# Kernel optimization log

Measured on AMD Instinct MI355X. Metric: run time of the kernel, lower is better.

## Reference

```python
import jax, jax.numpy as jnp
import numpy as np

BLOCK_SIZE = 64
WINDOW_SIZE = 256  # local_window pattern: each query block attends to blocks within the window
NEG_INF = -1e30


def setup_inputs() -> dict:
    key = jax.random.key(0)
    kq, kk, kv = jax.random.split(key, 3)
    B, S, H, D = 2, 4096, 16, 64
    q = jax.random.normal(kq, (B, S, H, D), dtype=jnp.float32)
    k = jax.random.normal(kk, (B, S, H, D), dtype=jnp.float32)
    v = jax.random.normal(kv, (B, S, H, D), dtype=jnp.float32)
    return {"q": q, "k": k, "v": v}


def _block_sparse_attn(q, k, v):
    # q, k, v: [B, S, H, D]
    B, S, H, D = q.shape
    bs = BLOCK_SIZE
    N = S // bs                      # number of blocks
    W = WINDOW_SIZE // bs            # window in blocks (4)
    half = W // 2
    offsets = jnp.arange(-half, half + 1)          # [K] neighbor offsets, K = W+1 = 5
    K = offsets.shape[0]

    i = jnp.arange(N)
    j = i[:, None] + offsets[None, :]              # [N, K] neighbor block ids
    valid = (j >= 0) & (j < N)                     # boundary mask
    jc = jnp.clip(j, 0, N - 1)

    # reshape into blocks: [B, H, N, bs, D]
    qb = q.reshape(B, N, bs, H, D).transpose(0, 3, 1, 2, 4)
    kb = k.reshape(B, N, bs, H, D).transpose(0, 3, 1, 2, 4)
    vb = v.reshape(B, N, bs, H, D).transpose(0, 3, 1, 2, 4)

    # gather only the active (neighbor) key/value blocks: [B, H, N, K, bs, D]
    kn = kb[:, :, jc]
    vn = vb[:, :, jc]

    scale = 1.0 / jnp.sqrt(jnp.asarray(D, dtype=q.dtype))
    # block scores: [B, H, N, bs, K, bs]
    scores = jnp.einsum('bhnqd,bhnkcd->bhnqkc', qb, kn) * scale
    scores = jnp.where(valid[None, None, :, None, :, None], scores, NEG_INF)

    # softmax over the union of active key blocks for each query block
    scores = scores.reshape(B, H, N, bs, K * bs)
    attn = jax.nn.softmax(scores, axis=-1)
    out = jnp.einsum('bhnqe,bhned->bhnqd', attn, vn.reshape(B, H, N, K * bs, D))

    # back to [B, S, H, D]
    return out.transpose(0, 2, 3, 1, 4).reshape(B, S, H, D)


def reference(q, k, v):
    return _block_sparse_attn(q, k, v)
```

## Files before the change

kernel.cpp:

```cpp
#include <hip/hip_runtime.h>

#define S_DIM 4096
#define H_DIM 16
#define D_DIM 64
#define N_BLK 64
#define NEG_INF_F (-1e30f)
#define QSCALE 0.125f

typedef __attribute__((ext_vector_type(4))) float f32x4;
typedef __attribute__((ext_vector_type(8))) short s16x8;
typedef __attribute__((ext_vector_type(4))) unsigned int u32x4;
typedef __attribute__((ext_vector_type(2))) unsigned int u32x2;

__device__ __forceinline__ unsigned int fbits(float f) {
    return __builtin_bit_cast(unsigned int, f);
}
__device__ __forceinline__ unsigned int pkbf(float a, float b) {
    return __builtin_amdgcn_perm(fbits(b) + 0x8000u, fbits(a) + 0x8000u, 0x07060302u);
}

__global__ __launch_bounds__(256, 2) void bsattn_kernel(
    const float* __restrict__ qg, const float* __restrict__ kg,
    const float* __restrict__ vg, float* __restrict__ outg)
{
    __shared__ unsigned int lds_vt[D_DIM * 256];

    const int tid  = threadIdx.x;
    const int w    = tid >> 6;
    const int lane = tid & 63;
    const int quad = lane >> 4;
    const int l16  = lane & 15;

    const int b  = blockIdx.z;
    const int h  = blockIdx.y;
    const int n0 = blockIdx.x << 2;
    const int n  = n0 + w;

    s16x8 bq[4][2];
#pragma unroll
    for (int qt = 0; qt < 4; ++qt) {
        const size_t qrow = ((size_t)(b * S_DIM + n * 64 + qt * 16 + l16) * H_DIM + h) * D_DIM;
#pragma unroll
        for (int hh = 0; hh < 2; ++hh) {
            const float4* qp = reinterpret_cast<const float4*>(qg + qrow + hh * 32 + quad * 8);
            float4 f0 = qp[0];
            float4 f1 = qp[1];
            u32x4 u;
            u.x = pkbf(f0.x * QSCALE, f0.y * QSCALE);
            u.y = pkbf(f0.z * QSCALE, f0.w * QSCALE);
            u.z = pkbf(f1.x * QSCALE, f1.y * QSCALE);
            u.w = pkbf(f1.z * QSCALE, f1.w * QSCALE);
            bq[qt][hh] = __builtin_bit_cast(s16x8, u);
        }
    }

    {
        const int jt = tid >> 5;
        const int sp = tid & 31;
        const int jv = n0 - 2 + jt;
        if (jv >= 0 && jv < N_BLK) {
            const float* v0p = vg + ((size_t)(b * S_DIM + jv * 64 + 2 * sp) * H_DIM + h) * D_DIM;
            const float* v1p = v0p + H_DIM * D_DIM;
            const int craw = jt * 64 + 2 * sp;
#pragma unroll
            for (int ch = 0; ch < 4; ++ch) {
                const int d0 = ch * 16;
                const float4* ap = reinterpret_cast<const float4*>(v0p + d0);
                const float4* bp = reinterpret_cast<const float4*>(v1p + d0);
                float4 a0 = ap[0], a1 = ap[1], a2 = ap[2], a3 = ap[3];
                float4 b0 = bp[0], b1 = bp[1], b2 = bp[2], b3 = bp[3];
                float av[16] = {a0.x,a0.y,a0.z,a0.w, a1.x,a1.y,a1.z,a1.w,
                                a2.x,a2.y,a2.z,a2.w, a3.x,a3.y,a3.z,a3.w};
                float bv[16] = {b0.x,b0.y,b0.z,b0.w, b1.x,b1.y,b1.z,b1.w,
                                b2.x,b2.y,b2.z,b2.w, b3.x,b3.y,b3.z,b3.w};
#pragma unroll
                for (int i = 0; i < 16; ++i) {
                    const int d = d0 + i;
                    lds_vt[d * 256 + (((craw + 8 * d) & 511) >> 1)] = pkbf(av[i], bv[i]);
                }
            }
        }
    }

    f32x4 o[4][4];
    float m_run[4], l_run[4];
#pragma unroll
    for (int qt = 0; qt < 4; ++qt) {
        m_run[qt] = NEG_INF_F; l_run[qt] = 0.f;
#pragma unroll
        for (int dt = 0; dt < 4; ++dt) o[qt][dt] = (f32x4){0.f, 0.f, 0.f, 0.f};
    }

    __syncthreads();

    const int colb = quad * 4 + 8 * l16;

    for (int t = 0; t < 5; ++t) {
        const int j = n - 2 + t;
        if (j < 0 || j >= N_BLK) continue;
        const int ji = w + t;

        float4 kf[4][2][2];
#pragma unroll
        for (int kt = 0; kt < 4; ++kt) {
            const size_t krow = ((size_t)(b * S_DIM + j * 64 + kt * 16 + l16) * H_DIM + h) * D_DIM + quad * 8;
#pragma unroll
            for (int hh = 0; hh < 2; ++hh) {
                const float4* kp = reinterpret_cast<const float4*>(kg + krow + hh * 32);
                kf[kt][hh][0] = kp[0];
                kf[kt][hh][1] = kp[1];
            }
        }
        s16x8 kbf[4][2];
#pragma unroll
        for (int kt = 0; kt < 4; ++kt)
#pragma unroll
            for (int hh = 0; hh < 2; ++hh) {
                u32x4 u;
                u.x = pkbf(kf[kt][hh][0].x, kf[kt][hh][0].y);
                u.y = pkbf(kf[kt][hh][0].z, kf[kt][hh][0].w);
                u.z = pkbf(kf[kt][hh][1].x, kf[kt][hh][1].y);
                u.w = pkbf(kf[kt][hh][1].z, kf[kt][hh][1].w);
                kbf[kt][hh] = __builtin_bit_cast(s16x8, u);
            }

        s16x8 pa[4][2];
#pragma unroll
        for (int qt = 0; qt < 4; ++qt) {
            f32x4 sa[4];
#pragma unroll
            for (int kt = 0; kt < 4; ++kt) {
                f32x4 z = {0.f, 0.f, 0.f, 0.f};
                f32x4 a0 = __builtin_amdgcn_mfma_f32_16x16x32_bf16(kbf[kt][0], bq[qt][0], z, 0, 0, 0);
                sa[kt]   = __builtin_amdgcn_mfma_f32_16x16x32_bf16(kbf[kt][1], bq[qt][1], a0, 0, 0, 0);
            }
            float mx = NEG_INF_F;
#pragma unroll
            for (int kt = 0; kt < 4; ++kt)
#pragma unroll
                for (int r = 0; r < 4; ++r) mx = fmaxf(mx, sa[kt][r]);
            mx = fmaxf(mx, __shfl_xor(mx, 16));
            mx = fmaxf(mx, __shfl_xor(mx, 32));
            const float mn = fmaxf(m_run[qt], mx);
            const float alpha = __expf(m_run[qt] - mn);
            m_run[qt] = mn;

            float rs = 0.f;
            unsigned int pk[4][2];
#pragma unroll
            for (int kt = 0; kt < 4; ++kt) {
                float e0 = __expf(sa[kt][0] - mn);
                float e1 = __expf(sa[kt][1] - mn);
                float e2 = __expf(sa[kt][2] - mn);
                float e3 = __expf(sa[kt][3] - mn);
                rs += (e0 + e1) + (e2 + e3);
                pk[kt][0] = pkbf(e0, e1);
                pk[kt][1] = pkbf(e2, e3);
            }
            rs += __shfl_xor(rs, 16);
            rs += __shfl_xor(rs, 32);
            l_run[qt] = l_run[qt] * alpha + rs;

            float ab[4];
#pragma unroll
            for (int r = 0; r < 4; ++r)
                ab[r] = __shfl(alpha, (lane & 48) + quad * 4 + r);
#pragma unroll
            for (int dt = 0; dt < 4; ++dt)
#pragma unroll
                for (int r = 0; r < 4; ++r) o[qt][dt][r] *= ab[r];

            pa[qt][0] = __builtin_bit_cast(s16x8, (u32x4){pk[0][0], pk[0][1], pk[1][0], pk[1][1]});
            pa[qt][1] = __builtin_bit_cast(s16x8, (u32x4){pk[2][0], pk[2][1], pk[3][0], pk[3][1]});
        }

        const int cb0 = ji * 64 + colb;
#pragma unroll
        for (int dt = 0; dt < 4; ++dt) {
            const int d = dt * 16 + l16;
            const unsigned int* vrow = lds_vt + d * 256;
            const int cb = cb0 + 128 * dt;
            u32x2 v00 = *reinterpret_cast<const u32x2*>(vrow + (((cb     ) & 511) >> 1));
            u32x2 v01 = *reinterpret_cast<const u32x2*>(vrow + (((cb + 16) & 511) >> 1));
            u32x2 v10 = *reinterpret_cast<const u32x2*>(vrow + (((cb + 32) & 511) >> 1));
            u32x2 v11 = *reinterpret_cast<const u32x2*>(vrow + (((cb + 48) & 511) >> 1));
            s16x8 vf0 = __builtin_bit_cast(s16x8, (u32x4){v00.x, v00.y, v01.x, v01.y});
            s16x8 vf1 = __builtin_bit_cast(s16x8, (u32x4){v10.x, v10.y, v11.x, v11.y});
#pragma unroll
            for (int qt = 0; qt < 4; ++qt) {
                o[qt][dt] = __builtin_amdgcn_mfma_f32_16x16x32_bf16(pa[qt][0], vf0, o[qt][dt], 0, 0, 0);
                o[qt][dt] = __builtin_amdgcn_mfma_f32_16x16x32_bf16(pa[qt][1], vf1, o[qt][dt], 0, 0, 0);
            }
        }
    }

#pragma unroll
    for (int qt = 0; qt < 4; ++qt) {
#pragma unroll
        for (int r = 0; r < 4; ++r) {
            const float lb = __shfl(l_run[qt], (lane & 48) + quad * 4 + r);
            const float inv = 1.0f / lb;
            const int row = n * 64 + qt * 16 + quad * 4 + r;
            float* op = outg + ((size_t)(b * S_DIM + row) * H_DIM + h) * D_DIM + l16;
#pragma unroll
            for (int dt = 0; dt < 4; ++dt)
                op[dt * 16] = o[qt][dt][r] * inv;
        }
    }
}

extern "C" void kernel_launch(void* const* d_in, const int* in_sizes, int n_in,
                              void* d_out, int out_size, void* d_ws, size_t ws_size,
                              hipStream_t stream) {
    const float* q = (const float*)d_in[0];
    const float* k = (const float*)d_in[1];
    const float* v = (const float*)d_in[2];
    float* out = (float*)d_out;
    const int B = in_sizes[0] / (S_DIM * H_DIM * D_DIM);
    dim3 grid(N_BLK / 4, H_DIM, B);
    dim3 block(256);
    hipLaunchKernelGGL(bsattn_kernel, grid, block, 0, stream, q, k, v, out);
}
```

Before: 159.7 us.

## Split each query block across two waves with 512-thread workgroups

Each workgroup now runs 8 waves instead of 4, and each pair of waves shares one 64-row query block, with each wave handling two of the four 16-row query tiles. The V-transpose staging into LDS is spread over twice as many threads. This halves per-wave accumulator registers and raises the number of waves in flight to improve latency hiding. In exchange, every K block is loaded from global memory and converted to bf16 twice, once by each wave of the pair, and the shared-memory footprint per workgroup is unchanged.

```diff
diff --git a/kernel.cpp b/kernel.cpp
--- a/kernel.cpp
+++ b/kernel.cpp
@@ -19,7 +19,7 @@
     return __builtin_amdgcn_perm(fbits(b) + 0x8000u, fbits(a) + 0x8000u, 0x07060302u);
 }
 
-__global__ __launch_bounds__(256, 2) void bsattn_kernel(
+__global__ __launch_bounds__(512, 4) void bsattn_kernel(
     const float* __restrict__ qg, const float* __restrict__ kg,
     const float* __restrict__ vg, float* __restrict__ outg)
 {
@@ -31,14 +31,16 @@
     const int quad = lane >> 4;
     const int l16  = lane & 15;
 
-    const int b  = blockIdx.z;
-    const int h  = blockIdx.y;
-    const int n0 = blockIdx.x << 2;
-    const int n  = n0 + w;
-
-    s16x8 bq[4][2];
-#pragma unroll
-    for (int qt = 0; qt < 4; ++qt) {
+    const int b   = blockIdx.z;
+    const int h   = blockIdx.y;
+    const int n0  = blockIdx.x << 2;
+    const int n   = n0 + (w >> 1);
+    const int qt0 = (w & 1) << 1;
+
+    s16x8 bq[2][2];
+#pragma unroll
+    for (int qq = 0; qq < 2; ++qq) {
+        const int qt = qt0 + qq;
         const size_t qrow = ((size_t)(b * S_DIM + n * 64 + qt * 16 + l16) * H_DIM + h) * D_DIM;
 #pragma unroll
         for (int hh = 0; hh < 2; ++hh) {
@@ -50,21 +52,22 @@
             u.y = pkbf(f0.z * QSCALE, f0.w * QSCALE);
             u.z = pkbf(f1.x * QSCALE, f1.y * QSCALE);
             u.w = pkbf(f1.z * QSCALE, f1.w * QSCALE);
-            bq[qt][hh] = __builtin_bit_cast(s16x8, u);
+            bq[qq][hh] = __builtin_bit_cast(s16x8, u);
         }
     }
 
     {
-        const int jt = tid >> 5;
-        const int sp = tid & 31;
+        const int jt = tid >> 6;
+        const int sp = (tid >> 1) & 31;
+        const int dh = tid & 1;
         const int jv = n0 - 2 + jt;
         if (jv >= 0 && jv < N_BLK) {
             const float* v0p = vg + ((size_t)(b * S_DIM + jv * 64 + 2 * sp) * H_DIM + h) * D_DIM;
             const float* v1p = v0p + H_DIM * D_DIM;
             const int craw = jt * 64 + 2 * sp;
 #pragma unroll
-            for (int ch = 0; ch < 4; ++ch) {
-                const int d0 = ch * 16;
+            for (int ch = 0; ch < 2; ++ch) {
+                const int d0 = dh * 32 + ch * 16;
                 const float4* ap = reinterpret_cast<const float4*>(v0p + d0);
                 const float4* bp = reinterpret_cast<const float4*>(v1p + d0);
                 float4 a0 = ap[0], a1 = ap[1], a2 = ap[2], a3 = ap[3];
@@ -82,13 +85,13 @@
         }
     }
 
-    f32x4 o[4][4];
-    float m_run[4], l_run[4];
-#pragma unroll
-    for (int qt = 0; qt < 4; ++qt) {
-        m_run[qt] = NEG_INF_F; l_run[qt] = 0.f;
-#pragma unroll
-        for (int dt = 0; dt < 4; ++dt) o[qt][dt] = (f32x4){0.f, 0.f, 0.f, 0.f};
+    f32x4 o[2][4];
+    float m_run[2], l_run[2];
+#pragma unroll
+    for (int qq = 0; qq < 2; ++qq) {
+        m_run[qq] = NEG_INF_F; l_run[qq] = 0.f;
+#pragma unroll
+        for (int dt = 0; dt < 4; ++dt) o[qq][dt] = (f32x4){0.f, 0.f, 0.f, 0.f};
     }
 
     __syncthreads();
@@ -98,7 +101,7 @@
     for (int t = 0; t < 5; ++t) {
         const int j = n - 2 + t;
         if (j < 0 || j >= N_BLK) continue;
-        const int ji = w + t;
+        const int ji = (w >> 1) + t;
 
         float4 kf[4][2][2];
 #pragma unroll
@@ -124,15 +127,15 @@
                 kbf[kt][hh] = __builtin_bit_cast(s16x8, u);
             }
 
-        s16x8 pa[4][2];
-#pragma unroll
-        for (int qt = 0; qt < 4; ++qt) {
+        s16x8 pa[2][2];
+#pragma unroll
+        for (int qq = 0; qq < 2; ++qq) {
             f32x4 sa[4];
 #pragma unroll
             for (int kt = 0; kt < 4; ++kt) {
                 f32x4 z = {0.f, 0.f, 0.f, 0.f};
-                f32x4 a0 = __builtin_amdgcn_mfma_f32_16x16x32_bf16(kbf[kt][0], bq[qt][0], z, 0, 0, 0);
-                sa[kt]   = __builtin_amdgcn_mfma_f32_16x16x32_bf16(kbf[kt][1], bq[qt][1], a0, 0, 0, 0);
+                f32x4 a0 = __builtin_amdgcn_mfma_f32_16x16x32_bf16(kbf[kt][0], bq[qq][0], z, 0, 0, 0);
+                sa[kt]   = __builtin_amdgcn_mfma_f32_16x16x32_bf16(kbf[kt][1], bq[qq][1], a0, 0, 0, 0);
             }
             float mx = NEG_INF_F;
 #pragma unroll
@@ -141,9 +144,9 @@
                 for (int r = 0; r < 4; ++r) mx = fmaxf(mx, sa[kt][r]);
             mx = fmaxf(mx, __shfl_xor(mx, 16));
             mx = fmaxf(mx, __shfl_xor(mx, 32));
-            const float mn = fmaxf(m_run[qt], mx);
-            const float alpha = __expf(m_run[qt] - mn);
-            m_run[qt] = mn;
+            const float mn = fmaxf(m_run[qq], mx);
+            const float alpha = __expf(m_run[qq] - mn);
+            m_run[qq] = mn;
 
             float rs = 0.f;
             unsigned int pk[4][2];
@@ -159,7 +162,7 @@
             }
             rs += __shfl_xor(rs, 16);
             rs += __shfl_xor(rs, 32);
-            l_run[qt] = l_run[qt] * alpha + rs;
+            l_run[qq] = l_run[qq] * alpha + rs;
 
             float ab[4];
 #pragma unroll
@@ -168,10 +171,10 @@
 #pragma unroll
             for (int dt = 0; dt < 4; ++dt)
 #pragma unroll
-                for (int r = 0; r < 4; ++r) o[qt][dt][r] *= ab[r];
-
-            pa[qt][0] = __builtin_bit_cast(s16x8, (u32x4){pk[0][0], pk[0][1], pk[1][0], pk[1][1]});
-            pa[qt][1] = __builtin_bit_cast(s16x8, (u32x4){pk[2][0], pk[2][1], pk[3][0], pk[3][1]});
+                for (int r = 0; r < 4; ++r) o[qq][dt][r] *= ab[r];
+
+            pa[qq][0] = __builtin_bit_cast(s16x8, (u32x4){pk[0][0], pk[0][1], pk[1][0], pk[1][1]});
+            pa[qq][1] = __builtin_bit_cast(s16x8, (u32x4){pk[2][0], pk[2][1], pk[3][0], pk[3][1]});
         }
 
         const int cb0 = ji * 64 + colb;
@@ -187,24 +190,25 @@
             s16x8 vf0 = __builtin_bit_cast(s16x8, (u32x4){v00.x, v00.y, v01.x, v01.y});
             s16x8 vf1 = __builtin_bit_cast(s16x8, (u32x4){v10.x, v10.y, v11.x, v11.y});
 #pragma unroll
-            for (int qt = 0; qt < 4; ++qt) {
-                o[qt][dt] = __builtin_amdgcn_mfma_f32_16x16x32_bf16(pa[qt][0], vf0, o[qt][dt], 0, 0, 0);
-                o[qt][dt] = __builtin_amdgcn_mfma_f32_16x16x32_bf16(pa[qt][1], vf1, o[qt][dt], 0, 0, 0);
-            }
-        }
-    }
-
-#pragma unroll
-    for (int qt = 0; qt < 4; ++qt) {
+            for (int qq = 0; qq < 2; ++qq) {
+                o[qq][dt] = __builtin_amdgcn_mfma_f32_16x16x32_bf16(pa[qq][0], vf0, o[qq][dt], 0, 0, 0);
+                o[qq][dt] = __builtin_amdgcn_mfma_f32_16x16x32_bf16(pa[qq][1], vf1, o[qq][dt], 0, 0, 0);
+            }
+        }
+    }
+
+#pragma unroll
+    for (int qq = 0; qq < 2; ++qq) {
+        const int qt = qt0 + qq;
 #pragma unroll
         for (int r = 0; r < 4; ++r) {
-            const float lb = __shfl(l_run[qt], (lane & 48) + quad * 4 + r);
+            const float lb = __shfl(l_run[qq], (lane & 48) + quad * 4 + r);
             const float inv = 1.0f / lb;
             const int row = n * 64 + qt * 16 + quad * 4 + r;
             float* op = outg + ((size_t)(b * S_DIM + row) * H_DIM + h) * D_DIM + l16;
 #pragma unroll
             for (int dt = 0; dt < 4; ++dt)
-                op[dt * 16] = o[qt][dt][r] * inv;
+                op[dt * 16] = o[qq][dt][r] * inv;
         }
     }
 }
@@ -218,6 +222,6 @@
     float* out = (float*)d_out;
     const int B = in_sizes[0] / (S_DIM * H_DIM * D_DIM);
     dim3 grid(N_BLK / 4, H_DIM, B);
-    dim3 block(256);
+    dim3 block(512);
     hipLaunchKernelGGL(bsattn_kernel, grid, block, 0, stream, q, k, v, out);
 }
```

Measured after the change: 199.0 us. 24.6% more time.

## Prefetch next K block into registers, lazily rescale softmax, add MFMA priority hints

Applied to the files above, without the earlier changes.

The global load of the next K block now starts before the current block's QK^T, softmax and PV work, software-pipelining the K fetch across loop iterations. The online softmax skips the rescale of the output accumulators and running sum unless the new max exceeds the stored max by more than 8, a threshold-based lazy rescale. s_setprio hints are placed around the MFMA bursts. This costs extra registers for the in-flight K block, may lower occupancy or cause spills, and relies on the exp values staying within bf16/fp32 range under the lazy-max bound.

```diff
diff --git a/kernel.cpp b/kernel.cpp
--- a/kernel.cpp
+++ b/kernel.cpp
@@ -19,6 +19,32 @@
     return __builtin_amdgcn_perm(fbits(b) + 0x8000u, fbits(a) + 0x8000u, 0x07060302u);
 }
 
+__device__ __forceinline__ void load_k(const float* __restrict__ kb, float4 (&kf)[4][2][2]) {
+#pragma unroll
+    for (int kt = 0; kt < 4; ++kt) {
+        const float4* kp = reinterpret_cast<const float4*>(kb + (size_t)kt * (16 * H_DIM * D_DIM));
+#pragma unroll
+        for (int hh = 0; hh < 2; ++hh) {
+            kf[kt][hh][0] = kp[hh * 8 + 0];
+            kf[kt][hh][1] = kp[hh * 8 + 1];
+        }
+    }
+}
+
+__device__ __forceinline__ void conv_k(const float4 (&kf)[4][2][2], s16x8 (&kbf)[4][2]) {
+#pragma unroll
+    for (int kt = 0; kt < 4; ++kt)
+#pragma unroll
+        for (int hh = 0; hh < 2; ++hh) {
+            u32x4 u;
+            u.x = pkbf(kf[kt][hh][0].x, kf[kt][hh][0].y);
+            u.y = pkbf(kf[kt][hh][0].z, kf[kt][hh][0].w);
+            u.z = pkbf(kf[kt][hh][1].x, kf[kt][hh][1].y);
+            u.w = pkbf(kf[kt][hh][1].z, kf[kt][hh][1].w);
+            kbf[kt][hh] = __builtin_bit_cast(s16x8, u);
+        }
+}
+
 __global__ __launch_bounds__(256, 2) void bsattn_kernel(
     const float* __restrict__ qg, const float* __restrict__ kg,
     const float* __restrict__ vg, float* __restrict__ outg)
@@ -35,6 +61,13 @@
     const int h  = blockIdx.y;
     const int n0 = blockIdx.x << 2;
     const int n  = n0 + w;
+
+    float4 kf[4][2][2];
+    s16x8 kbf[4][2];
+    {
+        int jc = n - 2; jc = jc < 0 ? 0 : jc;
+        load_k(kg + ((size_t)(b * S_DIM + jc * 64 + l16) * H_DIM + h) * D_DIM + quad * 8, kf);
+    }
 
     s16x8 bq[4][2];
 #pragma unroll
@@ -93,105 +126,103 @@
 
     __syncthreads();
 
+    conv_k(kf, kbf);
+
     const int colb = quad * 4 + 8 * l16;
 
+#pragma unroll 1
     for (int t = 0; t < 5; ++t) {
         const int j = n - 2 + t;
-        if (j < 0 || j >= N_BLK) continue;
-        const int ji = w + t;
-
-        float4 kf[4][2][2];
-#pragma unroll
-        for (int kt = 0; kt < 4; ++kt) {
-            const size_t krow = ((size_t)(b * S_DIM + j * 64 + kt * 16 + l16) * H_DIM + h) * D_DIM + quad * 8;
-#pragma unroll
-            for (int hh = 0; hh < 2; ++hh) {
-                const float4* kp = reinterpret_cast<const float4*>(kg + krow + hh * 32);
-                kf[kt][hh][0] = kp[0];
-                kf[kt][hh][1] = kp[1];
+
+        if (t < 4) {
+            int jn = j + 1;
+            jn = jn < 0 ? 0 : (jn > (N_BLK - 1) ? (N_BLK - 1) : jn);
+            load_k(kg + ((size_t)(b * S_DIM + jn * 64 + l16) * H_DIM + h) * D_DIM + quad * 8, kf);
+        }
+
+        if (j >= 0 && j < N_BLK) {
+            const int ji = w + t;
+
+            s16x8 pa[4][2];
+#pragma unroll
+            for (int qt = 0; qt < 4; ++qt) {
+                f32x4 sa[4];
+                __builtin_amdgcn_s_setprio(1);
+#pragma unroll
+                for (int kt = 0; kt < 4; ++kt) {
+                    f32x4 z = {0.f, 0.f, 0.f, 0.f};
+                    f32x4 a0 = __builtin_amdgcn_mfma_f32_16x16x32_bf16(kbf[kt][0], bq[qt][0], z, 0, 0, 0);
+                    sa[kt]   = __builtin_amdgcn_mfma_f32_16x16x32_bf16(kbf[kt][1], bq[qt][1], a0, 0, 0, 0);
+                }
+                __builtin_amdgcn_s_setprio(0);
+                float mx = NEG_INF_F;
+#pragma unroll
+                for (int kt = 0; kt < 4; ++kt)
+#pragma unroll
+                    for (int r = 0; r < 4; ++r) mx = fmaxf(mx, sa[kt][r]);
+                mx = fmaxf(mx, __shfl_xor(mx, 16));
+                mx = fmaxf(mx, __shfl_xor(mx, 32));
+
+                float mn = m_run[qt];
+                if (!__all(mx - mn <= 8.f)) {
+                    const float mnew = fmaxf(mn, mx);
+                    const float alpha = __expf(mn - mnew);
+                    float ab[4];
+#pragma unroll
+                    for (int r = 0; r < 4; ++r)
+                        ab[r] = __shfl(alpha, (lane & 48) + quad * 4 + r);
+#pragma unroll
+                    for (int dt = 0; dt < 4; ++dt)
+#pragma unroll
+                        for (int r = 0; r < 4; ++r) o[qt][dt][r] *= ab[r];
+                    l_run[qt] *= alpha;
+                    m_run[qt] = mnew;
+                    mn = mnew;
+                }
+
+                float rs = 0.f;
+                unsigned int pk[4][2];
+#pragma unroll
+                for (int kt = 0; kt < 4; ++kt) {
+                    float e0 = __expf(sa[kt][0] - mn);
+                    float e1 = __expf(sa[kt][1] - mn);
+                    float e2 = __expf(sa[kt][2] - mn);
+                    float e3 = __expf(sa[kt][3] - mn);
+                    rs += (e0 + e1) + (e2 + e3);
+                    pk[kt][0] = pkbf(e0, e1);
+                    pk[kt][1] = pkbf(e2, e3);
+                }
+                rs += __shfl_xor(rs, 16);
+                rs += __shfl_xor(rs, 32);
+                l_run[qt] += rs;
+
+                pa[qt][0] = __builtin_bit_cast(s16x8, (u32x4){pk[0][0], pk[0][1], pk[1][0], pk[1][1]});
+                pa[qt][1] = __builtin_bit_cast(s16x8, (u32x4){pk[2][0], pk[2][1], pk[3][0], pk[3][1]});
             }
-        }
-        s16x8 kbf[4][2];
-#pragma unroll
-        for (int kt = 0; kt < 4; ++kt)
-#pragma unroll
-            for (int hh = 0; hh < 2; ++hh) {
-                u32x4 u;
-                u.x = pkbf(kf[kt][hh][0].x, kf[kt][hh][0].y);
-                u.y = pkbf(kf[kt][hh][0].z, kf[kt][hh][0].w);
-                u.z = pkbf(kf[kt][hh][1].x, kf[kt][hh][1].y);
-                u.w = pkbf(kf[kt][hh][1].z, kf[kt][hh][1].w);
-                kbf[kt][hh] = __builtin_bit_cast(s16x8, u);
+
+            const int cb0 = ji * 64 + colb;
+#pragma unroll
+            for (int dt = 0; dt < 4; ++dt) {
+                const int d = dt * 16 + l16;
+                const unsigned int* vrow = lds_vt + d * 256;
+                const int cb = cb0 + 128 * dt;
+                u32x2 v00 = *reinterpret_cast<const u32x2*>(vrow + (((cb     ) & 511) >> 1));
+                u32x2 v01 = *reinterpret_cast<const u32x2*>(vrow + (((cb + 16) & 511) >> 1));
+                u32x2 v10 = *reinterpret_cast<const u32x2*>(vrow + (((cb + 32) & 511) >> 1));
+                u32x2 v11 = *reinterpret_cast<const u32x2*>(vrow + (((cb + 48) & 511) >> 1));
+                s16x8 vf0 = __builtin_bit_cast(s16x8, (u32x4){v00.x, v00.y, v01.x, v01.y});
+                s16x8 vf1 = __builtin_bit_cast(s16x8, (u32x4){v10.x, v10.y, v11.x, v11.y});
+                __builtin_amdgcn_s_setprio(1);
+#pragma unroll
+                for (int qt = 0; qt < 4; ++qt) {
+                    o[qt][dt] = __builtin_amdgcn_mfma_f32_16x16x32_bf16(pa[qt][0], vf0, o[qt][dt], 0, 0, 0);
+                    o[qt][dt] = __builtin_amdgcn_mfma_f32_16x16x32_bf16(pa[qt][1], vf1, o[qt][dt], 0, 0, 0);
+                }
+                __builtin_amdgcn_s_setprio(0);
             }
-
-        s16x8 pa[4][2];
-#pragma unroll
-        for (int qt = 0; qt < 4; ++qt) {
-            f32x4 sa[4];
-#pragma unroll
-            for (int kt = 0; kt < 4; ++kt) {
-                f32x4 z = {0.f, 0.f, 0.f, 0.f};
-                f32x4 a0 = __builtin_amdgcn_mfma_f32_16x16x32_bf16(kbf[kt][0], bq[qt][0], z, 0, 0, 0);
-                sa[kt]   = __builtin_amdgcn_mfma_f32_16x16x32_bf16(kbf[kt][1], bq[qt][1], a0, 0, 0, 0);
-            }
-            float mx = NEG_INF_F;
-#pragma unroll
-            for (int kt = 0; kt < 4; ++kt)
-#pragma unroll
-                for (int r = 0; r < 4; ++r) mx = fmaxf(mx, sa[kt][r]);
-            mx = fmaxf(mx, __shfl_xor(mx, 16));
-            mx = fmaxf(mx, __shfl_xor(mx, 32));
-            const float mn = fmaxf(m_run[qt], mx);
-            const float alpha = __expf(m_run[qt] - mn);
-            m_run[qt] = mn;
-
-            float rs = 0.f;
-            unsigned int pk[4][2];
-#pragma unroll
-            for (int kt = 0; kt < 4; ++kt) {
-                float e0 = __expf(sa[kt][0] - mn);
-                float e1 = __expf(sa[kt][1] - mn);
-                float e2 = __expf(sa[kt][2] - mn);
-                float e3 = __expf(sa[kt][3] - mn);
-                rs += (e0 + e1) + (e2 + e3);
-                pk[kt][0] = pkbf(e0, e1);
-                pk[kt][1] = pkbf(e2, e3);
-            }
-            rs += __shfl_xor(rs, 16);
-            rs += __shfl_xor(rs, 32);
-            l_run[qt] = l_run[qt] * alpha + rs;
-
-            float ab[4];
-#pragma unroll
-            for (int r = 0; r < 4; ++r)
-                ab[r] = __shfl(alpha, (lane & 48) + quad * 4 + r);
-#pragma unroll
-            for (int dt = 0; dt < 4; ++dt)
-#pragma unroll
-                for (int r = 0; r < 4; ++r) o[qt][dt][r] *= ab[r];
-
-            pa[qt][0] = __builtin_bit_cast(s16x8, (u32x4){pk[0][0], pk[0][1], pk[1][0], pk[1][1]});
-            pa[qt][1] = __builtin_bit_cast(s16x8, (u32x4){pk[2][0], pk[2][1], pk[3][0], pk[3][1]});
-        }
-
-        const int cb0 = ji * 64 + colb;
-#pragma unroll
-        for (int dt = 0; dt < 4; ++dt) {
-            const int d = dt * 16 + l16;
-            const unsigned int* vrow = lds_vt + d * 256;
-            const int cb = cb0 + 128 * dt;
-            u32x2 v00 = *reinterpret_cast<const u32x2*>(vrow + (((cb     ) & 511) >> 1));
-            u32x2 v01 = *reinterpret_cast<const u32x2*>(vrow + (((cb + 16) & 511) >> 1));
-            u32x2 v10 = *reinterpret_cast<const u32x2*>(vrow + (((cb + 32) & 511) >> 1));
-            u32x2 v11 = *reinterpret_cast<const u32x2*>(vrow + (((cb + 48) & 511) >> 1));
-            s16x8 vf0 = __builtin_bit_cast(s16x8, (u32x4){v00.x, v00.y, v01.x, v01.y});
-            s16x8 vf1 = __builtin_bit_cast(s16x8, (u32x4){v10.x, v10.y, v11.x, v11.y});
-#pragma unroll
-            for (int qt = 0; qt < 4; ++qt) {
-                o[qt][dt] = __builtin_amdgcn_mfma_f32_16x16x32_bf16(pa[qt][0], vf0, o[qt][dt], 0, 0, 0);
-                o[qt][dt] = __builtin_amdgcn_mfma_f32_16x16x32_bf16(pa[qt][1], vf1, o[qt][dt], 0, 0, 0);
-            }
-        }
+        }
+
+        if (t < 4) conv_k(kf, kbf);
     }
 
 #pragma unroll
```

After: 195.7 us. 1.23x slower.

## Split each query block's key window across two waves with LDS merge

Applied to the files above, without the earlier changes.

Each query block is now handled by two wavefronts instead of one: one processes key blocks 0-2 of the window and the other blocks 3-4, and the block grows to 512 threads. The partial softmax states (max, sum, and scaled outputs) are exchanged through LDS and merged, with each wave finalizing half of the query tiles. This doubles the wave count per workgroup to raise latency hiding and parallelism on a grid of only 512 workgroups. In exchange it adds extra barriers and LDS traffic, gives the two waves unequal work, and uses a higher per-block thread count that may limit registers per thread.

```diff
diff --git a/kernel.cpp b/kernel.cpp
--- a/kernel.cpp
+++ b/kernel.cpp
@@ -19,7 +19,7 @@
     return __builtin_amdgcn_perm(fbits(b) + 0x8000u, fbits(a) + 0x8000u, 0x07060302u);
 }
 
-__global__ __launch_bounds__(256, 2) void bsattn_kernel(
+__global__ __launch_bounds__(512, 2) void bsattn_kernel(
     const float* __restrict__ qg, const float* __restrict__ kg,
     const float* __restrict__ vg, float* __restrict__ outg)
 {
@@ -31,10 +31,12 @@
     const int quad = lane >> 4;
     const int l16  = lane & 15;
 
-    const int b  = blockIdx.z;
-    const int h  = blockIdx.y;
-    const int n0 = blockIdx.x << 2;
-    const int n  = n0 + w;
+    const int b    = blockIdx.z;
+    const int h    = blockIdx.y;
+    const int n0   = blockIdx.x << 2;
+    const int p    = w >> 1;
+    const int wsub = w & 1;
+    const int n    = n0 + p;
 
     s16x8 bq[4][2];
 #pragma unroll
@@ -55,16 +57,17 @@
     }
 
     {
-        const int jt = tid >> 5;
-        const int sp = tid & 31;
+        const int jt = w;
+        const int sp = lane & 31;
+        const int dh = lane >> 5;
         const int jv = n0 - 2 + jt;
         if (jv >= 0 && jv < N_BLK) {
             const float* v0p = vg + ((size_t)(b * S_DIM + jv * 64 + 2 * sp) * H_DIM + h) * D_DIM;
             const float* v1p = v0p + H_DIM * D_DIM;
             const int craw = jt * 64 + 2 * sp;
 #pragma unroll
-            for (int ch = 0; ch < 4; ++ch) {
-                const int d0 = ch * 16;
+            for (int ch = 0; ch < 2; ++ch) {
+                const int d0 = dh * 32 + ch * 16;
                 const float4* ap = reinterpret_cast<const float4*>(v0p + d0);
                 const float4* bp = reinterpret_cast<const float4*>(v1p + d0);
                 float4 a0 = ap[0], a1 = ap[1], a2 = ap[2], a3 = ap[3];
@@ -96,9 +99,10 @@
     const int colb = quad * 4 + 8 * l16;
 
     for (int t = 0; t < 5; ++t) {
+        if (wsub ? (t < 3) : (t >= 3)) continue;
         const int j = n - 2 + t;
         if (j < 0 || j >= N_BLK) continue;
-        const int ji = w + t;
+        const int ji = p + t;
 
         float4 kf[4][2][2];
 #pragma unroll
@@ -194,17 +198,78 @@
         }
     }
 
+    __syncthreads();
+    float* lbuf = reinterpret_cast<float*>(lds_vt);
+
+    if (quad == 0) {
+#pragma unroll
+        for (int qt = 0; qt < 4; ++qt) {
+            const int base = ((((p << 1) + wsub) * 4 + qt) * 16 + l16) * 2;
+            lbuf[base]     = m_run[qt];
+            lbuf[base + 1] = l_run[qt];
+        }
+    }
+    __syncthreads();
+
+    const int qm0 = wsub << 1;
+    float s_own[4];
+    float lmv[2];
 #pragma unroll
     for (int qt = 0; qt < 4; ++qt) {
+        const int pb = ((((p << 1) + (wsub ^ 1)) * 4 + qt) * 16 + l16) * 2;
+        const float mP = lbuf[pb], lP = lbuf[pb + 1];
+        const float mm = fmaxf(m_run[qt], mP);
+        s_own[qt] = __expf(m_run[qt] - mm);
+        const float lmt = l_run[qt] * s_own[qt] + lP * __expf(mP - mm);
+        if ((qt >> 1) == wsub) lmv[qt & 1] = lmt;
+    }
+    __syncthreads();
+
+    const int qo0 = (wsub ^ 1) << 1;
+#pragma unroll
+    for (int qq = 0; qq < 2; ++qq) {
+        const int qt = qo0 + qq;
+        float sr[4];
+#pragma unroll
+        for (int r = 0; r < 4; ++r)
+            sr[r] = __shfl(s_own[qt], (lane & 48) + quad * 4 + r);
+#pragma unroll
+        for (int dt = 0; dt < 4; ++dt) {
+            f32x4 sv;
+#pragma unroll
+            for (int r = 0; r < 4; ++r) sv[r] = o[qt][dt][r] * sr[r];
+            *reinterpret_cast<f32x4*>(lbuf + ((((p << 2) + qt) * 4 + dt) * 64 + lane) * 4) = sv;
+        }
+    }
+    __syncthreads();
+
+#pragma unroll
+    for (int qq = 0; qq < 2; ++qq) {
+        const int qt = qm0 + qq;
+        const float invl = 1.0f / lmv[qq];
+        float sr[4], ir[4];
 #pragma unroll
         for (int r = 0; r < 4; ++r) {
-            const float lb = __shfl(l_run[qt], (lane & 48) + quad * 4 + r);
-            const float inv = 1.0f / lb;
+            const int src = (lane & 48) + quad * 4 + r;
+            sr[r] = __shfl(s_own[qt], src);
+            ir[r] = __shfl(invl, src);
+        }
+        f32x4 res[4];
+#pragma unroll
+        for (int dt = 0; dt < 4; ++dt) {
+            const f32x4 oth = *reinterpret_cast<const f32x4*>(
+                lbuf + ((((p << 2) + qt) * 4 + dt) * 64 + lane) * 4);
+#pragma unroll
+            for (int r = 0; r < 4; ++r)
+                res[dt][r] = (o[qt][dt][r] * sr[r] + oth[r]) * ir[r];
+        }
+#pragma unroll
+        for (int r = 0; r < 4; ++r) {
             const int row = n * 64 + qt * 16 + quad * 4 + r;
             float* op = outg + ((size_t)(b * S_DIM + row) * H_DIM + h) * D_DIM + l16;
 #pragma unroll
             for (int dt = 0; dt < 4; ++dt)
-                op[dt * 16] = o[qt][dt][r] * inv;
+                op[dt * 16] = res[dt][r];
         }
     }
 }
@@ -218,6 +283,6 @@
     float* out = (float*)d_out;
     const int B = in_sizes[0] / (S_DIM * H_DIM * D_DIM);
     dim3 grid(N_BLK / 4, H_DIM, B);
-    dim3 block(256);
+    dim3 block(512);
     hipLaunchKernelGGL(bsattn_kernel, grid, block, 0, stream, q, k, v, out);
 }
```

After: 191.2 us. 19.8% more time.
